# Kernel tuning notes

Measured on AMD Instinct MI355X. Metric: run time of the kernel, lower is better.

The kernel has to match this reference:

```python
import jax, jax.numpy as jnp
import numpy as np

GAMMA = 0.5
EPS = 1e-06
REL_THRESH = 1e-09


def setup_inputs() -> dict:
    key = jax.random.key(0)
    k1, k2 = jax.random.split(key)
    B, T, D = 4, 4096, 256
    A_rel = jax.random.uniform(k1, (B, T, T), dtype=jnp.float32)
    # symmetrize as the docstring states A_rel is symmetric
    A_rel = 0.5 * (A_rel + jnp.swapaxes(A_rel, -1, -2))
    k_seq = jax.random.normal(k2, (B, T, D), dtype=jnp.float32)
    return {"A_rel": A_rel, "k_seq": k_seq}


def reference(A_rel, k_seq):
    # init_sequence: symmetric normalization W = D^{-1/2} A D^{-1/2}
    D = jnp.sum(A_rel, axis=-1) + EPS                  # (B, T)
    d_inv_sqrt = 1.0 / jnp.sqrt(D)                     # (B, T)
    W = A_rel * d_inv_sqrt[:, :, None] * d_inv_sqrt[:, None, :]  # (B, T, T)

    T = A_rel.shape[1]
    # step t uses W[:, t, :t+1] -> lower-triangular (incl. diagonal) causal mask
    tril = jnp.tril(jnp.ones((T, T), dtype=W.dtype))   # (T, T)
    W_causal = W * tril                                # (B, T, T)

    # a_t = sum_{s<=t} W[b,t,s] * k_s  for every t at once
    a = jnp.einsum('bts,bsd->btd', W_causal, k_seq)    # (B, T, D)

    # has_relation[b,t] = max_{s<=t} |W[b,t,s]| > 1e-9
    has_relation = jnp.max(jnp.abs(W) * tril, axis=-1) > REL_THRESH  # (B, T)

    a_scaled = a * jnp.sqrt(jnp.asarray(GAMMA, dtype=a.dtype))
    out = a_scaled * has_relation[:, :, None].astype(a_scaled.dtype)
    return out
```

## Files before the change

### kernel.cpp

```cpp
#include <hip/hip_runtime.h>
#include <hip/hip_bf16.h>

constexpr int Bn = 4;
constexpr int Tn = 4096;
constexpr int Dn = 256;
constexpr int NT = Tn / 64;
constexpr int NTRI = NT * (NT + 1) / 2;

using ushort = unsigned short;
typedef short short8 __attribute__((ext_vector_type(8)));
typedef float f32x4 __attribute__((ext_vector_type(4)));
typedef float f32x4v __attribute__((ext_vector_type(4)));

__device__ __forceinline__ ushort f2bu(float f) {
    __hip_bfloat16 h = __float2bfloat16(f);
    return __builtin_bit_cast(unsigned short, h);
}
__device__ __forceinline__ void gld_lds16(const ushort* g, ushort* l) {
    __builtin_amdgcn_global_load_lds((const __attribute__((address_space(1))) void*)g,
                                     (__attribute__((address_space(3))) void*)l,
                                     16, 0, 0);
}
__device__ __forceinline__ float dis_of(float a) { return rsqrtf(a + 1e-6f); }

__global__ __launch_bounds__(256) void tri_pass_kernel(
    const float* __restrict__ A, float* __restrict__ acc, ushort* __restrict__ Apk) {
    __shared__ float tile[64][68];
    int bid = blockIdx.x;
    int b = bid / NTRI;
    int r = bid - b * NTRI;
    int it = (int)((sqrtf(8.f * r + 1.f) - 1.f) * 0.5f);
    while ((it + 1) * (it + 2) / 2 <= r) ++it;
    while (it * (it + 1) / 2 > r) --it;
    int kt = r - it * (it + 1) / 2;
    int t0 = it * 64, s0 = kt * 64;
    bool diag = (kt == it);

    int tid = threadIdx.x;
    int i = tid >> 2;
    int c0 = (tid & 3) * 16;

    const float* g = A + ((size_t)(b * Tn + t0 + i) * Tn + s0 + c0);
    f32x4v v[4];
#pragma unroll
    for (int q = 0; q < 4; ++q) v[q] = __builtin_nontemporal_load((const f32x4v*)(g + 4 * q));

    float f[16];
#pragma unroll
    for (int q = 0; q < 4; ++q) {
        f[4 * q + 0] = v[q][0]; f[4 * q + 1] = v[q][1];
        f[4 * q + 2] = v[q][2]; f[4 * q + 3] = v[q][3];
    }
    float rp = 0.f;
#pragma unroll
    for (int e = 0; e < 16; ++e) rp += f[e];
    rp += __shfl_xor(rp, 1, 64);
    rp += __shfl_xor(rp, 2, 64);
    if ((tid & 3) == 0) atomicAdd(&acc[b * Tn + t0 + i], rp);

#pragma unroll
    for (int q = 0; q < 4; ++q) *(f32x4v*)&tile[i][c0 + 4 * q] = v[q];

    ushort* tb = Apk + (size_t)b * NTRI * 4096 + (size_t)(it * (it + 1) / 2 + kt) * 4096;
    unsigned w[8];
#pragma unroll
    for (int e = 0; e < 8; ++e) {
        float lo = f[2 * e], hi = f[2 * e + 1];
        if (diag) {
            if (c0 + 2 * e > i)     lo = 0.f;
            if (c0 + 2 * e + 1 > i) hi = 0.f;
        }
        w[e] = (unsigned)f2bu(lo) | ((unsigned)f2bu(hi) << 16);
    }
    *(uint4*)(tb + i * 64 + c0)     = make_uint4(w[0], w[1], w[2], w[3]);
    *(uint4*)(tb + i * 64 + c0 + 8) = make_uint4(w[4], w[5], w[6], w[7]);

    if (!diag) {
        __syncthreads();
        int j = tid & 63, p = tid >> 6;
        float cp = 0.f;
#pragma unroll
        for (int q = 0; q < 16; ++q) cp += tile[p * 16 + q][j];
        atomicAdd(&acc[b * Tn + s0 + j], cp);
    }
}

__global__ __launch_bounds__(256) void scale_transpose_kernel(
    const float* __restrict__ K, const float* __restrict__ acc, ushort* __restrict__ kT) {
    int bid = blockIdx.x;
    int b = bid >> 8;
    int rr = bid & 255;
    int st = rr >> 2, dt = rr & 3;
    int s0 = st * 64, d0 = dt * 64;
    __shared__ ushort tile[64][72];
    int tid = threadIdx.x;
#pragma unroll
    for (int q = 0; q < 2; ++q) {
        int idx = q * 256 + tid;
        int sl = idx >> 3, dl0 = (idx & 7) * 8;
        const float* g = K + ((size_t)(b * Tn + s0 + sl) * Dn + d0 + dl0);
        float sc = dis_of(acc[b * Tn + s0 + sl]);
        float4 v0 = *(const float4*)g;
        float4 v1 = *(const float4*)(g + 4);
        tile[sl][dl0 + 0] = f2bu(v0.x * sc);
        tile[sl][dl0 + 1] = f2bu(v0.y * sc);
        tile[sl][dl0 + 2] = f2bu(v0.z * sc);
        tile[sl][dl0 + 3] = f2bu(v0.w * sc);
        tile[sl][dl0 + 4] = f2bu(v1.x * sc);
        tile[sl][dl0 + 5] = f2bu(v1.y * sc);
        tile[sl][dl0 + 6] = f2bu(v1.z * sc);
        tile[sl][dl0 + 7] = f2bu(v1.w * sc);
    }
    __syncthreads();
#pragma unroll
    for (int q = 0; q < 2; ++q) {
        int idx = q * 256 + tid;
        int dl = idx >> 3, sl0 = (idx & 7) * 8;
        unsigned w[4];
#pragma unroll
        for (int e = 0; e < 4; ++e) {
            unsigned lo = tile[sl0 + 2 * e][dl];
            unsigned hi = tile[sl0 + 2 * e + 1][dl];
            w[e] = lo | (hi << 16);
        }
        *(uint4*)(kT + ((size_t)(b * Dn + d0 + dl) * Tn + s0 + sl0)) =
            make_uint4(w[0], w[1], w[2], w[3]);
    }
}

__global__ __launch_bounds__(256) void gemm_causal_kernel(
    const ushort* __restrict__ Apk, const ushort* __restrict__ kT,
    const float* __restrict__ acc_in, float* __restrict__ out,
    const ushort* __restrict__ zsrc) {
    __shared__ __attribute__((aligned(16))) ushort As[2][128 * 64];
    __shared__ __attribute__((aligned(16))) ushort Bs[2][64 * 64];
    __shared__ float rs[128];

    int bid = blockIdx.x;
    int g = bid >> 4;
    int sub = bid & 15;
    int it2 = (g < 16) ? (31 - g) : (g - 16);
    int b = sub >> 2;
    int d0 = (sub & 3) * 64;
    int itA = 2 * it2, itB = 2 * it2 + 1;
    int t0 = itA * 64;
    int nkt = 2 * it2 + 2;

    int tid = threadIdx.x;
    int lane = tid & 63;
    int w = tid >> 6;
    int l15 = lane & 15;

    const ushort* ApkA = Apk + (size_t)b * NTRI * 4096 + (size_t)(itA * (itA + 1) / 2) * 4096;
    const ushort* ApkB = Apk + (size_t)b * NTRI * 4096 + (size_t)(itB * (itB + 1) / 2) * 4096;
    const size_t kTbase = (size_t)(b * Dn + d0) * Tn;

    if (tid < 128) rs[tid] = 0.70710678118654752f * dis_of(acc_in[b * Tn + t0 + tid]);

    f32x4 acc[4][2];
#pragma unroll
    for (int mi = 0; mi < 4; ++mi)
#pragma unroll
        for (int ni = 0; ni < 2; ++ni) acc[mi][ni] = (f32x4){0.f, 0.f, 0.f, 0.f};

    int mrow = (w >> 1) * 64;
    int ncol = (w & 1) * 32;

    auto stage = [&](int buf, int kt) {
        bool lastA = (kt == itB);
        const ushort* baseA = ApkA + (size_t)kt * 4096;
        const ushort* baseB = ApkB + (size_t)kt * 4096;
#pragma unroll
        for (int q = 0; q < 4; ++q) {
            int idx = q * 256 + tid;
            int row = idx >> 3, ch = idx & 7;
            int sch = ((ch ^ (row & 7)) << 3);
            const ushort* src;
            if (row < 64) src = lastA ? zsrc : (baseA + row * 64 + sch);
            else          src = baseB + (size_t)(row - 64) * 64 + sch;
            gld_lds16(src, &As[buf][idx * 8]);
        }
#pragma unroll
        for (int q = 0; q < 2; ++q) {
            int idx = q * 256 + tid;
            int n = idx >> 3, ch = idx & 7;
            int sch = ((ch ^ (n & 7)) << 3);
            gld_lds16(kT + kTbase + (size_t)n * Tn + kt * 64 + sch, &Bs[buf][idx * 8]);
        }
    };

    stage(0, 0);
    __syncthreads();

    for (int kt = 0; kt < nkt; ++kt) {
        int cur = kt & 1;
        if (kt + 1 < nkt) stage(cur ^ 1, kt + 1);
#pragma unroll
        for (int ki = 0; ki < 2; ++ki) {
            int kch = ki * 4 + (lane >> 4);
            short8 af[4];
#pragma unroll
            for (int mi = 0; mi < 4; ++mi) {
                int rrow = mrow + 16 * mi + l15;
                af[mi] = *(const short8*)&As[cur][rrow * 64 + ((kch ^ (rrow & 7)) << 3)];
            }
            short8 bfr[2];
#pragma unroll
            for (int ni = 0; ni < 2; ++ni) {
                int n = ncol + 16 * ni + l15;
                bfr[ni] = *(const short8*)&Bs[cur][n * 64 + ((kch ^ (n & 7)) << 3)];
            }
#pragma unroll
            for (int mi = 0; mi < 4; ++mi)
#pragma unroll
                for (int ni = 0; ni < 2; ++ni)
                    acc[mi][ni] = __builtin_amdgcn_mfma_f32_16x16x32_bf16(
                        af[mi], bfr[ni], acc[mi][ni], 0, 0, 0);
        }
        __syncthreads();
    }

#pragma unroll
    for (int mi = 0; mi < 4; ++mi) {
#pragma unroll
        for (int ni = 0; ni < 2; ++ni) {
            int tl = mrow + 16 * mi + (lane >> 4) * 4;
            int d = d0 + ncol + 16 * ni + l15;
#pragma unroll
            for (int r = 0; r < 4; ++r) {
                int t = t0 + tl + r;
                out[(size_t)(b * Tn + t) * Dn + d] = acc[mi][ni][r] * rs[tl + r];
            }
        }
    }
}

extern "C" void kernel_launch(void* const* d_in, const int* in_sizes, int n_in,
                              void* d_out, int out_size, void* d_ws, size_t ws_size,
                              hipStream_t stream) {
    const float* A = (const float*)d_in[0];
    const float* K = (const float*)d_in[1];
    float* out = (float*)d_out;

    float* acc = (float*)d_ws;
    ushort* kT = (ushort*)(acc + Bn * Tn);
    ushort* Apk = kT + (size_t)Bn * Dn * Tn;
    ushort* zsrc = Apk + (size_t)Bn * NTRI * 4096;

    hipMemsetAsync(acc, 0, Bn * Tn * sizeof(float), stream);
    hipMemsetAsync(zsrc, 0, 256, stream);
    tri_pass_kernel<<<dim3(Bn * NTRI), dim3(256), 0, stream>>>(A, acc, Apk);
    scale_transpose_kernel<<<dim3(Bn * (Tn / 64) * (Dn / 64)), dim3(256), 0, stream>>>(K, acc, kT);
    gemm_causal_kernel<<<dim3(512), dim3(256), 0, stream>>>(Apk, kT, acc, out, zsrc);
}
```

Measured before the change: 403.0 us.

## Fuse bf16 packing of A into the causal GEMM's register-staged loads

The first pass no longer writes a packed, causally masked bf16 copy of A; it only computes row and column sums. The GEMM now reads fp32 A directly into registers one step ahead, applies the causal mask, converts to bf16 and writes to LDS after its MFMA work. This removes the intermediate bf16 write and read of A and its zero-source buffer. In exchange the GEMM reads fp32 A, twice the bytes per element, once per d-tile block (relying on cache for reuse), and the row-sum pass drops its nontemporal loads.

```diff
diff --git a/kernel.cpp b/kernel.cpp
--- a/kernel.cpp
+++ b/kernel.cpp
@@ -10,7 +10,6 @@
 using ushort = unsigned short;
 typedef short short8 __attribute__((ext_vector_type(8)));
 typedef float f32x4 __attribute__((ext_vector_type(4)));
-typedef float f32x4v __attribute__((ext_vector_type(4)));
 
 __device__ __forceinline__ ushort f2bu(float f) {
     __hip_bfloat16 h = __float2bfloat16(f);
@@ -23,8 +22,8 @@
 }
 __device__ __forceinline__ float dis_of(float a) { return rsqrtf(a + 1e-6f); }
 
-__global__ __launch_bounds__(256) void tri_pass_kernel(
-    const float* __restrict__ A, float* __restrict__ acc, ushort* __restrict__ Apk) {
+__global__ __launch_bounds__(256) void rowsum_kernel(
+    const float* __restrict__ A, float* __restrict__ acc) {
     __shared__ float tile[64][68];
     int bid = blockIdx.x;
     int b = bid / NTRI;
@@ -41,41 +40,20 @@
     int c0 = (tid & 3) * 16;
 
     const float* g = A + ((size_t)(b * Tn + t0 + i) * Tn + s0 + c0);
-    f32x4v v[4];
-#pragma unroll
-    for (int q = 0; q < 4; ++q) v[q] = __builtin_nontemporal_load((const f32x4v*)(g + 4 * q));
-
-    float f[16];
-#pragma unroll
-    for (int q = 0; q < 4; ++q) {
-        f[4 * q + 0] = v[q][0]; f[4 * q + 1] = v[q][1];
-        f[4 * q + 2] = v[q][2]; f[4 * q + 3] = v[q][3];
-    }
+    f32x4 v[4];
+#pragma unroll
+    for (int q = 0; q < 4; ++q) v[q] = *(const f32x4*)(g + 4 * q);
+
     float rp = 0.f;
 #pragma unroll
-    for (int e = 0; e < 16; ++e) rp += f[e];
+    for (int q = 0; q < 4; ++q) rp += v[q][0] + v[q][1] + v[q][2] + v[q][3];
     rp += __shfl_xor(rp, 1, 64);
     rp += __shfl_xor(rp, 2, 64);
     if ((tid & 3) == 0) atomicAdd(&acc[b * Tn + t0 + i], rp);
 
-#pragma unroll
-    for (int q = 0; q < 4; ++q) *(f32x4v*)&tile[i][c0 + 4 * q] = v[q];
-
-    ushort* tb = Apk + (size_t)b * NTRI * 4096 + (size_t)(it * (it + 1) / 2 + kt) * 4096;
-    unsigned w[8];
-#pragma unroll
-    for (int e = 0; e < 8; ++e) {
-        float lo = f[2 * e], hi = f[2 * e + 1];
-        if (diag) {
-            if (c0 + 2 * e > i)     lo = 0.f;
-            if (c0 + 2 * e + 1 > i) hi = 0.f;
-        }
-        w[e] = (unsigned)f2bu(lo) | ((unsigned)f2bu(hi) << 16);
-    }
-    *(uint4*)(tb + i * 64 + c0)     = make_uint4(w[0], w[1], w[2], w[3]);
-    *(uint4*)(tb + i * 64 + c0 + 8) = make_uint4(w[4], w[5], w[6], w[7]);
-
     if (!diag) {
+#pragma unroll
+        for (int q = 0; q < 4; ++q) *(f32x4*)&tile[i][c0 + 4 * q] = v[q];
         __syncthreads();
         int j = tid & 63, p = tid >> 6;
         float cp = 0.f;
@@ -128,10 +106,9 @@
     }
 }
 
-__global__ __launch_bounds__(256) void gemm_causal_kernel(
-    const ushort* __restrict__ Apk, const ushort* __restrict__ kT,
-    const float* __restrict__ acc_in, float* __restrict__ out,
-    const ushort* __restrict__ zsrc) {
+__global__ __launch_bounds__(256) void gemm_direct_kernel(
+    const float* __restrict__ A, const ushort* __restrict__ kT,
+    const float* __restrict__ acc_in, float* __restrict__ out) {
     __shared__ __attribute__((aligned(16))) ushort As[2][128 * 64];
     __shared__ __attribute__((aligned(16))) ushort Bs[2][64 * 64];
     __shared__ float rs[128];
@@ -142,8 +119,7 @@
     int it2 = (g < 16) ? (31 - g) : (g - 16);
     int b = sub >> 2;
     int d0 = (sub & 3) * 64;
-    int itA = 2 * it2, itB = 2 * it2 + 1;
-    int t0 = itA * 64;
+    int t0 = it2 * 128;
     int nkt = 2 * it2 + 2;
 
     int tid = threadIdx.x;
@@ -151,8 +127,6 @@
     int w = tid >> 6;
     int l15 = lane & 15;
 
-    const ushort* ApkA = Apk + (size_t)b * NTRI * 4096 + (size_t)(itA * (itA + 1) / 2) * 4096;
-    const ushort* ApkB = Apk + (size_t)b * NTRI * 4096 + (size_t)(itB * (itB + 1) / 2) * 4096;
     const size_t kTbase = (size_t)(b * Dn + d0) * Tn;
 
     if (tid < 128) rs[tid] = 0.70710678118654752f * dis_of(acc_in[b * Tn + t0 + tid]);
@@ -166,20 +140,38 @@
     int mrow = (w >> 1) * 64;
     int ncol = (w & 1) * 32;
 
-    auto stage = [&](int buf, int kt) {
-        bool lastA = (kt == itB);
-        const ushort* baseA = ApkA + (size_t)kt * 4096;
-        const ushort* baseB = ApkB + (size_t)kt * 4096;
-#pragma unroll
-        for (int q = 0; q < 4; ++q) {
-            int idx = q * 256 + tid;
-            int row = idx >> 3, ch = idx & 7;
-            int sch = ((ch ^ (row & 7)) << 3);
-            const ushort* src;
-            if (row < 64) src = lastA ? zsrc : (baseA + row * 64 + sch);
-            else          src = baseB + (size_t)(row - 64) * 64 + sch;
-            gld_lds16(src, &As[buf][idx * 8]);
-        }
+    f32x4 av[2][4];
+
+    auto a_issue = [&](int kt) {
+#pragma unroll
+        for (int p = 0; p < 2; ++p) {
+            int idx = p * 256 + tid;
+            int row = idx >> 2, aqc = idx & 3;
+            const float* gp = A + ((size_t)(b * Tn + t0 + row) * Tn + kt * 64 + aqc * 16);
+#pragma unroll
+            for (int q = 0; q < 4; ++q) av[p][q] = *(const f32x4*)(gp + 4 * q);
+        }
+    };
+    auto a_write = [&](int buf, int kt) {
+#pragma unroll
+        for (int p = 0; p < 2; ++p) {
+            int idx = p * 256 + tid;
+            int row = idx >> 2, aqc = idx & 3;
+            int keep = (t0 + row) - (kt * 64 + aqc * 16);
+            unsigned wv[8];
+#pragma unroll
+            for (int e = 0; e < 8; ++e) {
+                float lo = (2 * e     <= keep) ? av[p][(2 * e)     >> 2][(2 * e)     & 3] : 0.f;
+                float hi = (2 * e + 1 <= keep) ? av[p][(2 * e + 1) >> 2][(2 * e + 1) & 3] : 0.f;
+                wv[e] = (unsigned)f2bu(lo) | ((unsigned)f2bu(hi) << 16);
+            }
+            int ch0 = (aqc * 2) ^ (row & 7);
+            ushort* dst = &As[buf][row * 64];
+            *(uint4*)(dst + ch0 * 8)       = make_uint4(wv[0], wv[1], wv[2], wv[3]);
+            *(uint4*)(dst + (ch0 ^ 1) * 8) = make_uint4(wv[4], wv[5], wv[6], wv[7]);
+        }
+    };
+    auto b_issue = [&](int buf, int kt) {
 #pragma unroll
         for (int q = 0; q < 2; ++q) {
             int idx = q * 256 + tid;
@@ -188,27 +180,21 @@
             gld_lds16(kT + kTbase + (size_t)n * Tn + kt * 64 + sch, &Bs[buf][idx * 8]);
         }
     };
-
-    stage(0, 0);
-    __syncthreads();
-
-    for (int kt = 0; kt < nkt; ++kt) {
-        int cur = kt & 1;
-        if (kt + 1 < nkt) stage(cur ^ 1, kt + 1);
+    auto compute = [&](int buf) {
 #pragma unroll
         for (int ki = 0; ki < 2; ++ki) {
             int kch = ki * 4 + (lane >> 4);
             short8 af[4];
 #pragma unroll
             for (int mi = 0; mi < 4; ++mi) {
-                int rrow = mrow + 16 * mi + l15;
-                af[mi] = *(const short8*)&As[cur][rrow * 64 + ((kch ^ (rrow & 7)) << 3)];
+                int rr = mrow + 16 * mi + l15;
+                af[mi] = *(const short8*)&As[buf][rr * 64 + ((kch ^ (rr & 7)) << 3)];
             }
             short8 bfr[2];
 #pragma unroll
             for (int ni = 0; ni < 2; ++ni) {
                 int n = ncol + 16 * ni + l15;
-                bfr[ni] = *(const short8*)&Bs[cur][n * 64 + ((kch ^ (n & 7)) << 3)];
+                bfr[ni] = *(const short8*)&Bs[buf][n * 64 + ((kch ^ (n & 7)) << 3)];
             }
 #pragma unroll
             for (int mi = 0; mi < 4; ++mi)
@@ -217,6 +203,21 @@
                     acc[mi][ni] = __builtin_amdgcn_mfma_f32_16x16x32_bf16(
                         af[mi], bfr[ni], acc[mi][ni], 0, 0, 0);
         }
+    };
+
+    b_issue(0, 0);
+    a_issue(0);
+    a_write(0, 0);
+    __syncthreads();
+
+    for (int kt = 0; kt < nkt; ++kt) {
+        int cur = kt & 1;
+        if (kt + 1 < nkt) {
+            b_issue(cur ^ 1, kt + 1);
+            a_issue(kt + 1);
+        }
+        compute(cur);
+        if (kt + 1 < nkt) a_write(cur ^ 1, kt + 1);
         __syncthreads();
     }
 
@@ -244,12 +245,9 @@
 
     float* acc = (float*)d_ws;
     ushort* kT = (ushort*)(acc + Bn * Tn);
-    ushort* Apk = kT + (size_t)Bn * Dn * Tn;
-    ushort* zsrc = Apk + (size_t)Bn * NTRI * 4096;
 
     hipMemsetAsync(acc, 0, Bn * Tn * sizeof(float), stream);
-    hipMemsetAsync(zsrc, 0, 256, stream);
-    tri_pass_kernel<<<dim3(Bn * NTRI), dim3(256), 0, stream>>>(A, acc, Apk);
+    rowsum_kernel<<<dim3(Bn * NTRI), dim3(256), 0, stream>>>(A, acc);
     scale_transpose_kernel<<<dim3(Bn * (Tn / 64) * (Dn / 64)), dim3(256), 0, stream>>>(K, acc, kT);
-    gemm_causal_kernel<<<dim3(512), dim3(256), 0, stream>>>(Apk, kT, acc, out, zsrc);
-}
+    gemm_direct_kernel<<<dim3(512), dim3(256), 0, stream>>>(A, kT, acc, out);
+}
```

New measurement: 443.7 us. 10.1% more time.
